# Optimization experiments

Hardware: AMD Instinct MI355X
Metric: run time of the kernel (lower is better)

Reference implementation:

```python
import jax, jax.numpy as jnp
import numpy as np

B, T, NIN = 128, 256, 16
H1 = H2 = 512
NACT = 4
SLOPE = 25.0  # snntorch FastSigmoid default slope

@jax.custom_vjp
def spike(x):
    return (x > 0).astype(x.dtype)

def _spike_fwd(x):
    return (x > 0).astype(x.dtype), x

def _spike_bwd(x, g):
    # FastSigmoid surrogate: d/dx = 1 / (slope*|x| + 1)^2
    return (g / (SLOPE * jnp.abs(x) + 1.0) ** 2,)

spike.defvjp(_spike_fwd, _spike_bwd)

def setup_inputs() -> dict:
    key = jax.random.key(0)
    ks = jax.random.split(key, 12)
    def lin(k, fan_in, shape):
        lim = 1.0 / np.sqrt(fan_in)
        return jax.random.uniform(k, shape, jnp.float32, -lim, lim)
    return {
        "batch": jax.random.uniform(ks[0], (B, T, NIN), jnp.float32, 0.0, 2.5),
        "W1": lin(ks[1], NIN, (H1, NIN)), "b1": lin(ks[2], NIN, (H1,)),
        "beta1": jax.random.uniform(ks[3], (H1,), jnp.float32),
        "thr1": jax.random.uniform(ks[4], (H1,), jnp.float32),
        "W2": lin(ks[5], H1, (H2, H1)), "b2": lin(ks[6], H1, (H2,)),
        "beta2": jax.random.uniform(ks[7], (H2,), jnp.float32),
        "thr2": jax.random.uniform(ks[8], (H2,), jnp.float32),
        "Wa": lin(ks[9], H2, (NACT, H2)), "ba": lin(ks[10], H2, (NACT,)),
        "beta_act": jnp.float32(0.95),
        "inp_min": jnp.float32(0.0),
        "inp_max": jnp.float32(2.5),
    }

def _lif_subtract(cur, mem, beta, thr):
    # snntorch Leaky: reset from PRE-update membrane, detached; subtract reset
    reset = jax.lax.stop_gradient((mem - thr > 0).astype(mem.dtype))
    mem = jnp.clip(beta, 0.0, 1.0) * mem + cur - reset * thr
    return spike(mem - thr), mem

def reference(batch, W1, b1, beta1, thr1, W2, b2, beta2, thr2, Wa, ba, beta_act, inp_min, inp_max):
    Bb = batch.shape[0]
    x_seq = jnp.swapaxes(batch, 0, 1)  # [T, B, NIN]
    mem1 = jnp.zeros((Bb, W1.shape[0]), batch.dtype)
    mem2 = jnp.zeros((Bb, W2.shape[0]), batch.dtype)
    mem_a = jnp.zeros((Bb, Wa.shape[0]), batch.dtype)

    def step(carry, x):
        mem1, mem2, mem_a = carry
        x = (x - inp_min) / (inp_max - inp_min)
        spk1, mem1 = _lif_subtract(x @ W1.T + b1, mem1, beta1, thr1)
        spk2, mem2 = _lif_subtract(spk1 @ W2.T + b2, mem2, beta2, thr2)
        act = spk2 @ Wa.T + ba
        # action_lif: reset_mechanism='none', beta=0.95 learnable
        mem_a = jnp.clip(beta_act, 0.0, 1.0) * mem_a + act
        return (mem1, mem2, mem_a), mem_a.reshape(-1)  # torch: mem_act.reshape((1,-1))

    _, vals = jax.lax.scan(step, (mem1, mem2, mem_a), x_seq)
    # torch.stack(values, dim=1) of (1, B*NACT) tensors -> (1, T, B*NACT)
    return vals[None, :, :]
```

## Files before the change

kernel.cpp:

```cpp
#include <hip/hip_runtime.h>
#include <stdint.h>

typedef __attribute__((ext_vector_type(8))) short short8;
typedef __attribute__((ext_vector_type(4))) float f32x4;

#define T_STEPS 256
#define BATCH   128

#define LDS_BARRIER() asm volatile("s_waitcnt lgkmcnt(0)\n\ts_barrier" ::: "memory")

static __device__ inline unsigned short f2bf(float f) {
    unsigned int u = __float_as_uint(f);
    unsigned int r = u + 0x7FFFu + ((u >> 16) & 1u);
    return (unsigned short)(r >> 16);
}
static __device__ inline unsigned pack_hi16(unsigned a, unsigned b) {
    return __builtin_amdgcn_perm(b, a, 0x07060302u);
}
static __device__ inline void gload_lds16(const unsigned short* g, unsigned short* l) {
    __builtin_amdgcn_global_load_lds(
        (const __attribute__((address_space(1))) unsigned int*)(const void*)g,
        (__attribute__((address_space(3))) unsigned int*)(void*)l,
        16, 0, 0);
}

__global__ __launch_bounds__(256) void k_prep(
    const float* __restrict__ W2, const float* __restrict__ W1,
    const float* __restrict__ b1, const float* __restrict__ thr1,
    const float* __restrict__ imin_p, const float* __restrict__ imax_p,
    const float* __restrict__ batch,
    unsigned short* __restrict__ W2hi, unsigned short* __restrict__ W2lo,
    unsigned short* __restrict__ W1rows, float* __restrict__ b1s,
    unsigned short* __restrict__ Xf)
{
    int blk = blockIdx.x, tid = threadIdx.x;
    if (blk < 256) {
        int gid = blk * 256 + tid;
        f32x4 wv = *(const f32x4*)(W2 + (size_t)gid * 4);
        unsigned short hi[4], lo[4];
#pragma unroll
        for (int e = 0; e < 4; ++e) {
            float wf = wv[e];
            unsigned short h = f2bf(wf);
            float hf = __uint_as_float(((unsigned int)h) << 16);
            hi[e] = h;
            lo[e] = f2bf(wf - hf);
        }
        uint2 ph, pl;
        ph.x = (unsigned)hi[0] | ((unsigned)hi[1] << 16);
        ph.y = (unsigned)hi[2] | ((unsigned)hi[3] << 16);
        pl.x = (unsigned)lo[0] | ((unsigned)lo[1] << 16);
        pl.y = (unsigned)lo[2] | ((unsigned)lo[3] << 16);
        *(uint2*)(W2hi + (size_t)gid * 4) = ph;
        *(uint2*)(W2lo + (size_t)gid * 4) = pl;
    } else if (blk < 258) {
        int h = (blk - 256) * 256 + tid;
        float wsc = 1.0f / thr1[h];
        unsigned short row[64];
#pragma unroll
        for (int k = 0; k < 16; ++k) {
            float wv = W1[h * 16 + k] * wsc;
            unsigned a = __float_as_uint(wv) & 0xFFFF0000u;
            float r1 = wv - __uint_as_float(a);
            unsigned m = __float_as_uint(r1) & 0xFFFF0000u;
            float r2 = r1 - __uint_as_float(m);
            unsigned l = __float_as_uint(r2) & 0xFFFF0000u;
            row[k]      = (unsigned short)(a >> 16);
            row[16 + k] = (unsigned short)(m >> 16);
            row[32 + k] = (unsigned short)(l >> 16);
            row[48 + k] = 0;
        }
        b1s[h] = b1[h] * wsc;
        uint4* dst = (uint4*)(W1rows + (size_t)h * 64);
#pragma unroll
        for (int i = 0; i < 8; ++i) dst[i] = ((uint4*)row)[i];
    } else {
        int gid    = (blk - 258) * 256 + tid;
        int lane32 = gid & 31;
        int btile  = (gid >> 5) & 7;
        int t      = gid >> 8;
        int q1 = lane32 >> 4, m15 = lane32 & 15;
        int b  = btile * 16 + m15;
        float imin = imin_p[0];
        float isc  = 1.0f / (imax_p[0] - imin);
        const float* xp = batch + ((size_t)b * T_STEPS + t) * 16 + q1 * 8;
        unsigned uh[8], um[8], ul[8];
#pragma unroll
        for (int j = 0; j < 8; ++j) {
            float xv = (xp[j] - imin) * isc;
            unsigned a = __float_as_uint(xv) & 0xFFFF0000u;
            float r1 = xv - __uint_as_float(a);
            unsigned m = __float_as_uint(r1) & 0xFFFF0000u;
            float r2 = r1 - __uint_as_float(m);
            unsigned l = __float_as_uint(r2) & 0xFFFF0000u;
            uh[j] = a; um[j] = m; ul[j] = l;
        }
        uint4 XH, XM, XL;
        XH.x = pack_hi16(uh[0], uh[1]); XH.y = pack_hi16(uh[2], uh[3]);
        XH.z = pack_hi16(uh[4], uh[5]); XH.w = pack_hi16(uh[6], uh[7]);
        XM.x = pack_hi16(um[0], um[1]); XM.y = pack_hi16(um[2], um[3]);
        XM.z = pack_hi16(um[4], um[5]); XM.w = pack_hi16(um[6], um[7]);
        XL.x = pack_hi16(ul[0], ul[1]); XL.y = pack_hi16(ul[2], ul[3]);
        XL.z = pack_hi16(ul[4], ul[5]); XL.w = pack_hi16(ul[6], ul[7]);
        unsigned short* dst = Xf + ((size_t)t * 8 + btile) * 1024 + lane32 * 8;
        *(uint4*)(dst +   0) = XH;
        *(uint4*)(dst + 256) = XM;
        *(uint4*)(dst + 512) = XL;
    }
}

union XF { uint4 u; short8 s; };

__global__ __launch_bounds__(1024, 4) void k_main(
    const unsigned short* __restrict__ Xf,
    const unsigned short* __restrict__ W2hi, const unsigned short* __restrict__ W2lo,
    const unsigned short* __restrict__ W1rows, const float* __restrict__ b1s,
    const float* __restrict__ beta1, const float* __restrict__ b2,
    const float* __restrict__ beta2, const float* __restrict__ thr2,
    unsigned short* __restrict__ spkbits)
{
    __shared__ float Cbuf[8][4096];
    __shared__ unsigned short Xs[8192];

    int tid  = threadIdx.x;
    int lane = tid & 63;
    int w    = tid >> 6;
    int q = lane >> 4, m15 = lane & 15;
    int btile = blockIdx.x & 7;
    int slice = blockIdx.x >> 3;

    short8 A1[2], A2[2], A3[2];
#pragma unroll
    for (int c = 0; c < 2; ++c) {
        const unsigned short* rp = W1rows + (size_t)(w * 32 + c * 16 + m15) * 64;
        A1[c] = *(const short8*)(rp + q * 8);
        A2[c] = *(const short8*)(rp + q * 8 + (q >> 1) * 16);
        A3[c] = *(const short8*)(rp + 16 + q * 8);
    }
    int jg = slice * 16 + m15;
    short8 bhi, blo;
    {
        const unsigned short* ph = W2hi + (size_t)jg * 512 + w * 32 + q * 4;
        const unsigned short* pl = W2lo + (size_t)jg * 512 + w * 32 + q * 4;
        uint2 h0 = *(const uint2*)(ph);
        uint2 h1 = *(const uint2*)(ph + 16);
        uint2 l0 = *(const uint2*)(pl);
        uint2 l1 = *(const uint2*)(pl + 16);
        union { uint4 u; short8 s; } tb;
        tb.u.x = h0.x; tb.u.y = h0.y; tb.u.z = h1.x; tb.u.w = h1.y;
        bhi = tb.s;
        tb.u.x = l0.x; tb.u.y = l0.y; tb.u.z = l1.x; tb.u.w = l1.y;
        blo = tb.s;
    }

    f32x4 b14[2], bet1[2];
#pragma unroll
    for (int c = 0; c < 2; ++c) {
        int h0 = w * 32 + c * 16 + q * 4;
        b14[c] = *(const f32x4*)(b1s + h0);
        f32x4 bb = *(const f32x4*)(beta1 + h0);
#pragma unroll
        for (int r = 0; r < 4; ++r) bet1[c][r] = fminf(fmaxf(bb[r], 0.0f), 1.0f);
    }
    float m1[8], spk1f[8];
#pragma unroll
    for (int i = 0; i < 8; ++i) { m1[i] = 0.0f; spk1f[i] = 0.0f; }

    float beta2r = fminf(fmaxf(beta2[jg], 0.0f), 1.0f);
    float thr2r  = thr2[jg];
    float nthr2  = -thr2r;
    float b2r    = b2[jg];
    float m2 = 0.0f, spk2f = 0.0f;

    const unsigned short* xgbase = Xf + (size_t)btile * 1024 + (size_t)lane * 8;
    int l31x8 = (lane & 31) * 8;
    int o1 = l31x8;
    int o2 = l31x8 + 256;
    int o3 = l31x8 + (lane < 32 ? 512 : 0);
    int o4 = l31x8 + (lane < 32 ? 512 : 256);

    if (w == 15) {
#pragma unroll
        for (int s = 0; s < 5; ++s) {
            gload_lds16(xgbase + (size_t)s * 8192,       Xs + s * 1024);
            gload_lds16(xgbase + (size_t)s * 8192 + 512, Xs + s * 1024 + 512);
        }
        asm volatile("s_waitcnt vmcnt(0)" ::: "memory");
    }
    __syncthreads();

    XF xc[4], xn[4];
    {
        const unsigned short* s = Xs;
        xc[0].u = *(const uint4*)(s + o1);
        xc[1].u = *(const uint4*)(s + o2);
        xc[2].u = *(const uint4*)(s + o3);
        xc[3].u = *(const uint4*)(s + o4);
    }
    __syncthreads();

    auto reduce_one = [&](int slot, int step) __attribute__((always_inline)) {
        float cur2 = b2r;
#pragma unroll
        for (int wp = 0; wp < 16; ++wp) cur2 += Cbuf[slot][w * 1024 + wp * 64 + lane];
        m2 = fmaf(beta2r, m2, cur2);
        m2 = fmaf(spk2f, nthr2, m2);
        bool sp2 = m2 > thr2r;
        spk2f = sp2 ? 1.0f : 0.0f;
        unsigned long long mask = __ballot(sp2);
        if (lane < 4) {
            unsigned short v = (unsigned short)(mask >> (lane * 16));
            spkbits[((size_t)step * BATCH + btile * 16 + lane * 4 + w) * 32 + slice] = v;
        }
    };

    auto gbody = [&](int ts, int k, XF* xcur, XF* xnx) __attribute__((always_inline)) {
        {
            const unsigned short* sx = Xs + ((k + 1) & 7) * 1024;
            xnx[0].u = *(const uint4*)(sx + o1);
            xnx[1].u = *(const uint4*)(sx + o2);
            xnx[2].u = *(const uint4*)(sx + o3);
            xnx[3].u = *(const uint4*)(sx + o4);
        }
        f32x4 D[2];
#pragma unroll
        for (int c = 0; c < 2; ++c) {
            D[c] = __builtin_amdgcn_mfma_f32_16x16x32_bf16(A1[c], xcur[0].s, b14[c], 0, 0, 0);
            D[c] = __builtin_amdgcn_mfma_f32_16x16x32_bf16(A1[c], xcur[1].s, D[c], 0, 0, 0);
            D[c] = __builtin_amdgcn_mfma_f32_16x16x32_bf16(A2[c], xcur[2].s, D[c], 0, 0, 0);
            D[c] = __builtin_amdgcn_mfma_f32_16x16x32_bf16(A3[c], xcur[3].s, D[c], 0, 0, 0);
        }
#pragma unroll
        for (int i = 0; i < 8; ++i) {
            int c = i >> 2, r = i & 3;
            float mv = fmaf(bet1[c][r], m1[i], D[c][r]);
            mv -= spk1f[i];
            bool sp = mv > 1.0f;
            m1[i] = mv;
            spk1f[i] = sp ? 1.0f : 0.0f;
        }
        union { uint4 u; short8 s; } af;
        af.u.x = pack_hi16(__float_as_uint(spk1f[0]), __float_as_uint(spk1f[1]));
        af.u.y = pack_hi16(__float_as_uint(spk1f[2]), __float_as_uint(spk1f[3]));
        af.u.z = pack_hi16(__float_as_uint(spk1f[4]), __float_as_uint(spk1f[5]));
        af.u.w = pack_hi16(__float_as_uint(spk1f[6]), __float_as_uint(spk1f[7]));
        f32x4 C2 = { 0.f, 0.f, 0.f, 0.f };
        C2 = __builtin_amdgcn_mfma_f32_16x16x32_bf16(af.s, bhi, C2, 0, 0, 0);
        C2 = __builtin_amdgcn_mfma_f32_16x16x32_bf16(af.s, blo, C2, 0, 0, 0);
        float* cb = Cbuf[k & 7];
#pragma unroll
        for (int r = 0; r < 4; ++r)
            cb[r * 1024 + w * 64 + lane] = C2[r];
    };

    auto group = [&](int ts, int G) __attribute__((always_inline)) {
        if (w == 15) {
#pragma unroll
            for (int i = 0; i < 4; ++i) {
                int s = ts + G + 5 + i; if (s > T_STEPS - 1) s = T_STEPS - 1;
                const unsigned short* g = xgbase + (size_t)s * 8192;
                unsigned short* l = Xs + ((G + 5 + i) & 7) * 1024;
                gload_lds16(g,       l);
                gload_lds16(g + 512, l + 512);
            }
        }
        if (w < 4 && (ts + G >= 4)) {
#pragma unroll
            for (int i = 0; i < 4; ++i)
                reduce_one((G + 4 + i) & 7, ts + G - 4 + i);
        }
        gbody(ts, G + 0, xc, xn);
        gbody(ts, G + 1, xn, xc);
        gbody(ts, G + 2, xc, xn);
        gbody(ts, G + 3, xn, xc);
        if (w == 15) asm volatile("s_waitcnt vmcnt(0)" ::: "memory");
        LDS_BARRIER();
    };

#pragma unroll 1
    for (int ts = 0; ts < T_STEPS; ts += 8) {
        group(ts, 0);
        group(ts, 4);
    }
    if (w < 4) {
#pragma unroll
        for (int i = 0; i < 4; ++i)
            reduce_one(4 + i, T_STEPS - 4 + i);
    }
}

__global__ __launch_bounds__(512) void k_act(
    const unsigned short* __restrict__ spkbits,
    const float* __restrict__ Wa, const float* __restrict__ ba,
    const float* __restrict__ beta_act_p, float* __restrict__ out,
    f32x4* __restrict__ Lws, f32x4* __restrict__ Cws)
{
    __shared__ f32x4 waT[512];
    __shared__ f32x4 part[512];
    __shared__ f32x4 sc[128];
    int tid = threadIdx.x;
    int b   = blockIdx.x & 127;
    int c   = blockIdx.x >> 7;
    int tl  = tid & 127;
    int s   = tid >> 7;
    int t   = c * 128 + tl;

    {
        f32x4 v = { Wa[tid], Wa[512 + tid], Wa[1024 + tid], Wa[1536 + tid] };
        waT[tid] = v;
    }
    float bact = fminf(fmaxf(beta_act_p[0], 0.0f), 1.0f);
    f32x4 acc;
    if (s == 0) { acc[0] = ba[0]; acc[1] = ba[1]; acc[2] = ba[2]; acc[3] = ba[3]; }
    else        { acc[0] = 0.f;   acc[1] = 0.f;   acc[2] = 0.f;   acc[3] = 0.f;   }
    __syncthreads();

    const unsigned short* sp = spkbits + ((size_t)t * BATCH + b) * 32 + s * 8;
    uint4 v = *(const uint4*)sp;
    unsigned int wbuf[4] = { v.x, v.y, v.z, v.w };
#pragma unroll
    for (int ww = 0; ww < 4; ++ww) {
#pragma unroll
        for (int half = 0; half < 2; ++half) {
            unsigned int wd = (wbuf[ww] >> (half * 16)) & 0xFFFFu;
            int seg = s * 8 + ww * 2 + half;
#pragma unroll
            for (int i = 0; i < 16; ++i) {
                float sel = ((wd >> i) & 1u) ? 1.0f : 0.0f;
                f32x4 wv = waT[seg * 16 + i];
                acc[0] = fmaf(sel, wv[0], acc[0]);
                acc[1] = fmaf(sel, wv[1], acc[1]);
                acc[2] = fmaf(sel, wv[2], acc[2]);
                acc[3] = fmaf(sel, wv[3], acc[3]);
            }
        }
    }
    part[tid] = acc;
    __syncthreads();
    if (tid < 128) {
        f32x4 a0 = part[tid], a1 = part[tid + 128], a2 = part[tid + 256], a3 = part[tid + 384];
        f32x4 sum;
        sum[0] = ((a0[0] + a1[0]) + a2[0]) + a3[0];
        sum[1] = ((a0[1] + a1[1]) + a2[1]) + a3[1];
        sum[2] = ((a0[2] + a1[2]) + a2[2]) + a3[2];
        sum[3] = ((a0[3] + a1[3]) + a2[3]) + a3[3];
        sc[tid] = sum;
    }
    __syncthreads();
    float bd = bact;
    for (int d = 1; d < 128; d <<= 1) {
        f32x4 cv = { 0.f, 0.f, 0.f, 0.f }, pv = { 0.f, 0.f, 0.f, 0.f };
        if (tid < 128) {
            cv = sc[tid];
            if (tid >= d) pv = sc[tid - d];
        }
        __syncthreads();
        if (tid < 128) {
            cv[0] = fmaf(bd, pv[0], cv[0]);
            cv[1] = fmaf(bd, pv[1], cv[1]);
            cv[2] = fmaf(bd, pv[2], cv[2]);
            cv[3] = fmaf(bd, pv[3], cv[3]);
            sc[tid] = cv;
        }
        __syncthreads();
        bd *= bd;
    }
    if (tid < 128) {
        f32x4 res = sc[tid];
        if (c == 0) {
            *(f32x4*)(out + (size_t)t * 512 + b * 4) = res;
            if (tl == 127) Cws[b] = res;
        } else {
            Lws[b * 128 + tl] = res;
        }
    }
}

__global__ __launch_bounds__(128) void k_act2(
    const f32x4* __restrict__ Lws, const f32x4* __restrict__ Cws,
    const float* __restrict__ beta_act_p, float* __restrict__ out)
{
    int tl = threadIdx.x;
    int b  = blockIdx.x;
    float bact = fminf(fmaxf(beta_act_p[0], 0.0f), 1.0f);
    float p = 1.0f, base = bact;
    int e = tl + 1;
#pragma unroll
    for (int i = 0; i < 8; ++i) { if (e & 1) p *= base; base *= base; e >>= 1; }
    f32x4 L = Lws[b * 128 + tl];
    f32x4 C = Cws[b];
    f32x4 r;
    r[0] = fmaf(p, C[0], L[0]);
    r[1] = fmaf(p, C[1], L[1]);
    r[2] = fmaf(p, C[2], L[2]);
    r[3] = fmaf(p, C[3], L[3]);
    *(f32x4*)(out + (size_t)(128 + tl) * 512 + b * 4) = r;
}

extern "C" void kernel_launch(void* const* d_in, const int* in_sizes, int n_in,
                              void* d_out, int out_size, void* d_ws, size_t ws_size,
                              hipStream_t stream)
{
    const float* batch    = (const float*)d_in[0];
    const float* W1       = (const float*)d_in[1];
    const float* b1       = (const float*)d_in[2];
    const float* beta1    = (const float*)d_in[3];
    const float* thr1     = (const float*)d_in[4];
    const float* W2       = (const float*)d_in[5];
    const float* b2       = (const float*)d_in[6];
    const float* beta2    = (const float*)d_in[7];
    const float* thr2     = (const float*)d_in[8];
    const float* Wa       = (const float*)d_in[9];
    const float* ba       = (const float*)d_in[10];
    const float* beta_act = (const float*)d_in[11];
    const float* inp_min  = (const float*)d_in[12];
    const float* inp_max  = (const float*)d_in[13];
    float* out            = (float*)d_out;

    char* ws = (char*)d_ws;
    unsigned short* W2hi    = (unsigned short*)ws;
    unsigned short* W2lo    = (unsigned short*)(ws + (512u << 10));
    unsigned short* W1rows  = (unsigned short*)(ws + (1u << 20));
    float*          b1s     = (float*)(ws + (1u << 20) + (64u << 10));
    unsigned short* Xf      = (unsigned short*)(ws + (2u << 20));
    f32x4*          Lws     = (f32x4*)(ws + (6u << 20));
    f32x4*          Cws     = (f32x4*)(ws + (6u << 20) + (256u << 10));
    unsigned short* spkbits = (unsigned short*)(ws + (10u << 20));

    hipLaunchKernelGGL(k_prep, dim3(514), dim3(256), 0, stream,
                       W2, W1, b1, thr1, inp_min, inp_max, batch,
                       W2hi, W2lo, W1rows, b1s, Xf);
    hipLaunchKernelGGL(k_main, dim3(256), dim3(1024), 0, stream,
                       Xf, W2hi, W2lo, W1rows, b1s, beta1, b2, beta2, thr2, spkbits);
    hipLaunchKernelGGL(k_act, dim3(256), dim3(512), 0, stream,
                       spkbits, Wa, ba, beta_act, out, Lws, Cws);
    hipLaunchKernelGGL(k_act2, dim3(128), dim3(128), 0, stream, Lws, Cws, beta_act, out);
}
```

Before: 319.0 us.

## Barrier every two timesteps instead of four and halve the Cbuf ring

Reworks the main recurrent loop so that one workgroup barrier covers two timesteps instead of four. The layer-2 partial-sum ring buffer shrinks from 8 slots to 4, and the input prefetch depth drops from 5 to 4 steps. The smaller LDS footprint could raise occupancy and the reduction lag is shorter, but twice as many barriers are executed and reducer waves have less slack to overlap with the MFMA work. The initial post-load __syncthreads is also removed.

Result: faster. 258.4 us, median of 2 (-19.0%).

```diff
diff --git a/kernel.cpp b/kernel.cpp
--- a/kernel.cpp
+++ b/kernel.cpp
@@ -119,7 +119,7 @@
     const float* __restrict__ beta2, const float* __restrict__ thr2,
     unsigned short* __restrict__ spkbits)
 {
-    __shared__ float Cbuf[8][4096];
+    __shared__ float Cbuf[4][4096];
     __shared__ unsigned short Xs[8192];
 
     int tid  = threadIdx.x;
@@ -181,7 +181,7 @@
 
     if (w == 15) {
 #pragma unroll
-        for (int s = 0; s < 5; ++s) {
+        for (int s = 0; s < 4; ++s) {
             gload_lds16(xgbase + (size_t)s * 8192,       Xs + s * 1024);
             gload_lds16(xgbase + (size_t)s * 8192 + 512, Xs + s * 1024 + 512);
         }
@@ -197,7 +197,6 @@
         xc[2].u = *(const uint4*)(s + o3);
         xc[3].u = *(const uint4*)(s + o4);
     }
-    __syncthreads();
 
     auto reduce_one = [&](int slot, int step) __attribute__((always_inline)) {
         float cur2 = b2r;
@@ -214,9 +213,9 @@
         }
     };
 
-    auto gbody = [&](int ts, int k, XF* xcur, XF* xnx) __attribute__((always_inline)) {
+    auto body = [&](int step, XF* xcur, XF* xnx) __attribute__((always_inline)) {
         {
-            const unsigned short* sx = Xs + ((k + 1) & 7) * 1024;
+            const unsigned short* sx = Xs + (size_t)(((step + 1) & 7) * 1024);
             xnx[0].u = *(const uint4*)(sx + o1);
             xnx[1].u = *(const uint4*)(sx + o2);
             xnx[2].u = *(const uint4*)(sx + o3);
@@ -247,45 +246,39 @@
         f32x4 C2 = { 0.f, 0.f, 0.f, 0.f };
         C2 = __builtin_amdgcn_mfma_f32_16x16x32_bf16(af.s, bhi, C2, 0, 0, 0);
         C2 = __builtin_amdgcn_mfma_f32_16x16x32_bf16(af.s, blo, C2, 0, 0, 0);
-        float* cb = Cbuf[k & 7];
+        float* cb = Cbuf[step & 3];
 #pragma unroll
         for (int r = 0; r < 4; ++r)
             cb[r * 1024 + w * 64 + lane] = C2[r];
     };
 
-    auto group = [&](int ts, int G) __attribute__((always_inline)) {
+#pragma unroll 1
+    for (int p = 0; p < T_STEPS / 2; ++p) {
+        int s0 = p << 1;
         if (w == 15) {
-#pragma unroll
-            for (int i = 0; i < 4; ++i) {
-                int s = ts + G + 5 + i; if (s > T_STEPS - 1) s = T_STEPS - 1;
-                const unsigned short* g = xgbase + (size_t)s * 8192;
-                unsigned short* l = Xs + ((G + 5 + i) & 7) * 1024;
-                gload_lds16(g,       l);
-                gload_lds16(g + 512, l + 512);
-            }
-        }
-        if (w < 4 && (ts + G >= 4)) {
-#pragma unroll
-            for (int i = 0; i < 4; ++i)
-                reduce_one((G + 4 + i) & 7, ts + G - 4 + i);
-        }
-        gbody(ts, G + 0, xc, xn);
-        gbody(ts, G + 1, xn, xc);
-        gbody(ts, G + 2, xc, xn);
-        gbody(ts, G + 3, xn, xc);
+            int ta = s0 + 4; if (ta > T_STEPS - 1) ta = T_STEPS - 1;
+            int tb = s0 + 5; if (tb > T_STEPS - 1) tb = T_STEPS - 1;
+            const unsigned short* ga = xgbase + (size_t)ta * 8192;
+            const unsigned short* gb = xgbase + (size_t)tb * 8192;
+            unsigned short* la = Xs + (size_t)(((s0 + 4) & 7) * 1024);
+            unsigned short* lb = Xs + (size_t)(((s0 + 5) & 7) * 1024);
+            gload_lds16(ga,       la);
+            gload_lds16(ga + 512, la + 512);
+            gload_lds16(gb,       lb);
+            gload_lds16(gb + 512, lb + 512);
+        }
+        if (w < 4 && p > 0) {
+            reduce_one((s0 + 2) & 3, s0 - 2);
+            reduce_one((s0 + 3) & 3, s0 - 1);
+        }
+        body(s0,     xc, xn);
+        body(s0 + 1, xn, xc);
         if (w == 15) asm volatile("s_waitcnt vmcnt(0)" ::: "memory");
         LDS_BARRIER();
-    };
-
-#pragma unroll 1
-    for (int ts = 0; ts < T_STEPS; ts += 8) {
-        group(ts, 0);
-        group(ts, 4);
     }
     if (w < 4) {
-#pragma unroll
-        for (int i = 0; i < 4; ++i)
-            reduce_one(4 + i, T_STEPS - 4 + i);
+        reduce_one(2, T_STEPS - 2);
+        reduce_one(3, T_STEPS - 1);
     }
 }
 
```
